# Performance work log

Hardware: AMD Instinct MI355X
Metric: run time of the kernel (lower is better)

## Reference

```python
import jax, jax.numpy as jnp
import numpy as np

B = 1024      # total windows (batch*windows_per_image)
W = 7         # window_size
T = W * W     # tokens per window = 49
C = 256       # scaled_emb_dim = emb_dim * 2**level
H = 8         # heads
D = C // H    # head_dim = 32
NUM_POS = 2 * W - 1


def _relative_pos():
    coords = np.arange(W)
    coords = np.stack(np.meshgrid(coords, coords, indexing='ij')).reshape(2, -1)
    rp = coords[:, :, None] - coords[:, None, :] + (W - 1)
    return jnp.asarray(rp, dtype=jnp.int32)  # (2, T, T)


def setup_inputs() -> dict:
    key = jax.random.key(0)
    ks = jax.random.split(key, 12)
    s = 0.02
    return {
        'x': jax.random.normal(ks[0], (B, T, C), dtype=jnp.float32),
        'relative_pos': _relative_pos(),
        'bias_table': jax.random.truncated_normal(ks[1], -2.0, 2.0, (H, NUM_POS, NUM_POS), dtype=jnp.float32) * s,
        'wq': jax.random.normal(ks[2], (C, H, D), dtype=jnp.float32) / np.sqrt(C),
        'bq': jnp.zeros((H, D), dtype=jnp.float32),
        'wk': jax.random.normal(ks[3], (C, H, D), dtype=jnp.float32) / np.sqrt(C),
        'bk': jnp.zeros((H, D), dtype=jnp.float32),
        'wv': jax.random.normal(ks[4], (C, H, D), dtype=jnp.float32) / np.sqrt(C),
        'bv': jnp.zeros((H, D), dtype=jnp.float32),
        'wo': jax.random.normal(ks[5], (H, D, C), dtype=jnp.float32) / np.sqrt(C),
        'bo': jnp.zeros((C,), dtype=jnp.float32),
        'dw': jax.random.normal(ks[6], (C, C), dtype=jnp.float32) / np.sqrt(C),
        'db': jnp.zeros((C,), dtype=jnp.float32),
    }


def reference(x, relative_pos, bias_table, wq, bq, wk, bk, wv, bv, wo, bo, dw, db):
    # QKV projections (flax DenseGeneral with bias)
    q = jnp.einsum('btc,chd->bthd', x, wq) + bq  # (B,T,H,D)
    k = jnp.einsum('btc,chd->bthd', x, wk) + bk
    v = jnp.einsum('btc,chd->bthd', x, wv) + bv

    # gathered relative position bias: (H, T, T)
    bias = bias_table[:, relative_pos[0], relative_pos[1]]

    # attention logits with query scaling (flax dot_product_attention)
    q = q / jnp.sqrt(jnp.asarray(D, dtype=q.dtype))
    logits = jnp.einsum('bqhd,bkhd->bhqk', q, k) + bias[None]
    attn = jax.nn.softmax(logits, axis=-1)

    out = jnp.einsum('bhqk,bkhd->bqhd', attn, v)
    y = jnp.einsum('bqhd,hdc->bqc', out, wo) + bo  # attention out projection
    y = jnp.einsum('btc,cf->btf', y, dw) + db      # trailing Dense(scaled_emb_dim)
    return y
```

## Files before the change

kernel.cpp:

```cpp
#include <hip/hip_runtime.h>
#include <stdint.h>

#define T 49
#define CCH 256

typedef __bf16 bf16x8 __attribute__((ext_vector_type(8)));
typedef float f32x4 __attribute__((ext_vector_type(4)));

static __device__ __forceinline__ unsigned short f2bf(float f){
  __bf16 h = (__bf16)f;
  return __builtin_bit_cast(unsigned short, h);
}
static __device__ __forceinline__ float bf2f(unsigned short h){
  return __builtin_bit_cast(float, ((uint32_t)h) << 16);
}
static __device__ __forceinline__ uint32_t pk2(float a, float b){
  return (uint32_t)f2bf(a) | ((uint32_t)f2bf(b) << 16);
}
static __device__ __forceinline__ f32x4 mfma16(bf16x8 a, bf16x8 b, f32x4 c){
  return __builtin_amdgcn_mfma_f32_16x16x32_bf16(a, b, c, 0, 0, 0);
}
#define SWZ(row) ((((row) & 7) << 4))

static __device__ __forceinline__ bf16x8 build_frag(uint32_t lo_w0, uint32_t lo_w1,
                                                    uint32_t hi_w0, uint32_t hi_w1,
                                                    int srcA, int srcB, bool use_hi){
  uint32_t a0 = (uint32_t)__shfl((int)lo_w0, srcA, 64);
  uint32_t c0 = (uint32_t)__shfl((int)hi_w0, srcA, 64);
  uint32_t a1 = (uint32_t)__shfl((int)lo_w1, srcA, 64);
  uint32_t c1 = (uint32_t)__shfl((int)hi_w1, srcA, 64);
  uint32_t a2 = (uint32_t)__shfl((int)lo_w0, srcB, 64);
  uint32_t c2 = (uint32_t)__shfl((int)hi_w0, srcB, 64);
  uint32_t a3 = (uint32_t)__shfl((int)lo_w1, srcB, 64);
  uint32_t c3 = (uint32_t)__shfl((int)hi_w1, srcB, 64);
  uint4 u = use_hi ? make_uint4(c0, c1, c2, c3) : make_uint4(a0, a1, a2, a3);
  return __builtin_bit_cast(bf16x8, u);
}


__global__ void prep_wqkvT(const float* __restrict__ wq, const float* __restrict__ wk,
                           const float* __restrict__ wv, unsigned short* __restrict__ out){
  int bk = blockIdx.x;
  int p = bk >> 8, kk = bk & 255;
  int n = threadIdx.x;
  const float* w = (p == 0) ? wq : (p == 1 ? wk : wv);
  float scl = (p == 0) ? 0.17677669529663687f : 1.0f;
  out[(size_t)(p * 256 + n) * 256 + kk] = f2bf(w[kk * 256 + n] * scl);
}

__global__ void prep_wodT(const float* __restrict__ wo, const float* __restrict__ dw,
                          unsigned short* __restrict__ out){
  int hd = blockIdx.x;
  int c = threadIdx.x;
  float s = 0.f;
  for (int cp = 0; cp < 256; ++cp) s = fmaf(wo[hd * 256 + cp], dw[cp * 256 + c], s);
  out[(size_t)c * 256 + hd] = f2bf(s);
}

__global__ void prep_misc(const int* __restrict__ rp, const float* __restrict__ btab,
                          const float* __restrict__ bq, const float* __restrict__ bk,
                          const float* __restrict__ bv, const float* __restrict__ bo,
                          const float* __restrict__ dwm, const float* __restrict__ db,
                          unsigned short* __restrict__ biasP, float* __restrict__ bqkv,
                          float* __restrict__ bod){
  int t = threadIdx.x;
  if (blockIdx.x == 0){
    for (int idx = t; idx < 768; idx += 256){
      int p = idx >> 8, n = idx & 255;
      float v = (p == 0) ? bq[n] * 0.17677669529663687f : (p == 1 ? bk[n] : bv[n]);
      bqkv[idx] = v;
    }
    float s = db[t];
    for (int cp = 0; cp < 256; ++cp) s = fmaf(bo[cp], dwm[cp * 256 + t], s);
    bod[t] = s;
  } else {
    int h = blockIdx.x - 1;
    for (int idx = t; idx < 4096; idx += 256){
      int r  = idx & 3;
      int lo = (idx >> 2) & 15;
      int g  = (idx >> 6) & 3;
      int nt = (idx >> 8) & 3;
      int jt = idx >> 10;
      int j = 16 * jt + 4 * g + r;
      int i = 16 * nt + lo;
      float v;
      if (j >= T) v = -1e30f;
      else if (i >= T) v = 0.f;
      else {
        int r0 = rp[i * 49 + j];
        int r1 = rp[2401 + i * 49 + j];
        v = btab[h * 169 + r0 * 13 + r1];
      }
      biasP[h * 4096 + idx] = f2bf(v);
    }
  }
}

__launch_bounds__(512, 4)
__global__ void wmsa_main(const float* __restrict__ x,
                          const unsigned short* __restrict__ wqkvT,
                          const unsigned short* __restrict__ wodT,
                          const unsigned short* __restrict__ biasP,
                          const float* __restrict__ bqkv,
                          const float* __restrict__ bod,
                          float* __restrict__ y){
  __shared__ unsigned short xs[64 * 256];
  __shared__ unsigned short vts[8 * 32 * 64];

  const int b    = blockIdx.x;
  const int tid  = threadIdx.x;
  const int h    = tid >> 6;
  const int lane = tid & 63;
  const int g    = lane >> 4;
  const int lo   = lane & 15;
  char* xs_c = (char*)xs;

  const float* xb = x + (size_t)b * T * CCH;
  {
    float4 vv[8];
    #pragma unroll
    for (int k2 = 0; k2 < 8; ++k2){
      int idx = tid + k2 * 512;
      int row = idx >> 6, c4 = idx & 63;
      vv[k2] = make_float4(0.f, 0.f, 0.f, 0.f);
      if (row < T) vv[k2] = reinterpret_cast<const float4*>(xb)[row * 64 + c4];
    }
    #pragma unroll
    for (int k2 = 0; k2 < 8; ++k2){
      int idx = tid + k2 * 512;
      int row = idx >> 6, c4 = idx & 63;
      *reinterpret_cast<uint2*>(xs_c + row * 512 + ((c4 * 8) ^ SWZ(row)))
          = make_uint2(pk2(vv[k2].x, vv[k2].y), pk2(vv[k2].z, vv[k2].w));
    }
  }
  __syncthreads();

  const int  srcA = lo + 16 * ((2 * g) & 3);
  const int  srcB = lo + 16 * ((2 * g + 1) & 3);
  const bool ghi  = (g >= 2);

  {
    f32x4 avc[4][2];
    #pragma unroll
    for (int mt = 0; mt < 4; ++mt)
      #pragma unroll
      for (int nt = 0; nt < 2; ++nt) avc[mt][nt] = f32x4{0,0,0,0};

    #pragma unroll 1
    for (int kb = 0; kb < 2; ++kb){
      bf16x8 wv[2][4];
      #pragma unroll
      for (int nt = 0; nt < 2; ++nt)
        #pragma unroll
        for (int q4 = 0; q4 < 4; ++q4)
          wv[nt][q4] = *reinterpret_cast<const bf16x8*>(
              wqkvT + (size_t)(512 + h * 32 + 16 * nt + lo) * 256 + (kb * 4 + q4) * 32 + 8 * g);
      #pragma unroll
      for (int q4 = 0; q4 < 4; ++q4){
        int kt = kb * 4 + q4;
        bf16x8 ax[4];
        #pragma unroll
        for (int mt = 0; mt < 4; ++mt){
          int row = 16 * mt + lo;
          ax[mt] = *reinterpret_cast<const bf16x8*>(xs_c + row * 512 + ((kt * 64 + 16 * g) ^ SWZ(row)));
        }
        #pragma unroll
        for (int nt = 0; nt < 2; ++nt)
          #pragma unroll
          for (int mt = 0; mt < 4; ++mt) avc[mt][nt] = mfma16(ax[mt], wv[nt][q4], avc[mt][nt]);
      }
    }
    #pragma unroll
    for (int nt = 0; nt < 2; ++nt){
      const float bvs = bqkv[512 + h * 32 + 16 * nt + lo];
      const int d = 16 * nt + lo;
      #pragma unroll
      for (int mt = 0; mt < 4; ++mt){
        f32x4 t = avc[mt][nt];
        *reinterpret_cast<uint2*>((char*)vts + h * 4096 + d * 128 + ((mt * 32 + g * 8) ^ SWZ(d)))
            = make_uint2(pk2(t[0] + bvs, t[1] + bvs), pk2(t[2] + bvs, t[3] + bvs));
      }
    }
  }

  bf16x8 fk[4];
  {
    f32x4 akk[2][4];
    #pragma unroll
    for (int mt = 0; mt < 2; ++mt)
      #pragma unroll
      for (int nt = 0; nt < 4; ++nt) akk[mt][nt] = f32x4{0,0,0,0};

    #pragma unroll 1
    for (int kb = 0; kb < 2; ++kb){
      bf16x8 wk[2][4];
      #pragma unroll
      for (int mt = 0; mt < 2; ++mt)
        #pragma unroll
        for (int q4 = 0; q4 < 4; ++q4)
          wk[mt][q4] = *reinterpret_cast<const bf16x8*>(
              wqkvT + (size_t)(256 + h * 32 + 16 * mt + lo) * 256 + (kb * 4 + q4) * 32 + 8 * g);
      #pragma unroll
      for (int q4 = 0; q4 < 4; ++q4){
        int kt = kb * 4 + q4;
        bf16x8 bx[4];
        #pragma unroll
        for (int nt = 0; nt < 4; ++nt){
          int row = 16 * nt + lo;
          bx[nt] = *reinterpret_cast<const bf16x8*>(xs_c + row * 512 + ((kt * 64 + 16 * g) ^ SWZ(row)));
        }
        #pragma unroll
        for (int mt = 0; mt < 2; ++mt)
          #pragma unroll
          for (int nt = 0; nt < 4; ++nt) akk[mt][nt] = mfma16(wk[mt][q4], bx[nt], akk[mt][nt]);
      }
    }
    uint32_t pkk[2][4][2];
    #pragma unroll
    for (int mt = 0; mt < 2; ++mt){
      const float4 b4k = *reinterpret_cast<const float4*>(bqkv + 256 + h * 32 + 16 * mt + 4 * g);
      #pragma unroll
      for (int nt = 0; nt < 4; ++nt){
        f32x4 tk = akk[mt][nt];
        tk[0] += b4k.x; tk[1] += b4k.y; tk[2] += b4k.z; tk[3] += b4k.w;
        pkk[mt][nt][0] = pk2(tk[0], tk[1]); pkk[mt][nt][1] = pk2(tk[2], tk[3]);
      }
    }
    #pragma unroll
    for (int nt = 0; nt < 4; ++nt)
      fk[nt] = build_frag(pkk[0][nt][0], pkk[0][nt][1], pkk[1][nt][0], pkk[1][nt][1], srcA, srcB, ghi);
  }

  bf16x8 fq[4];
  {
    f32x4 aq[2][4];
    #pragma unroll
    for (int mt = 0; mt < 2; ++mt)
      #pragma unroll
      for (int nt = 0; nt < 4; ++nt) aq[mt][nt] = f32x4{0,0,0,0};

    #pragma unroll 1
    for (int kb = 0; kb < 4; ++kb){
      bf16x8 wq2[2][2];
      #pragma unroll
      for (int mt = 0; mt < 2; ++mt)
        #pragma unroll
        for (int q2 = 0; q2 < 2; ++q2)
          wq2[mt][q2] = *reinterpret_cast<const bf16x8*>(
              wqkvT + (size_t)(h * 32 + 16 * mt + lo) * 256 + (kb * 2 + q2) * 32 + 8 * g);
      #pragma unroll
      for (int q2 = 0; q2 < 2; ++q2){
        int kt = kb * 2 + q2;
        bf16x8 bx[4];
        #pragma unroll
        for (int nt = 0; nt < 4; ++nt){
          int row = 16 * nt + lo;
          bx[nt] = *reinterpret_cast<const bf16x8*>(xs_c + row * 512 + ((kt * 64 + 16 * g) ^ SWZ(row)));
        }
        #pragma unroll
        for (int mt = 0; mt < 2; ++mt)
          #pragma unroll
          for (int nt = 0; nt < 4; ++nt) aq[mt][nt] = mfma16(wq2[mt][q2], bx[nt], aq[mt][nt]);
      }
    }
    uint32_t pq[2][4][2];
    #pragma unroll
    for (int mt = 0; mt < 2; ++mt){
      const float4 b4q = *reinterpret_cast<const float4*>(bqkv + h * 32 + 16 * mt + 4 * g);
      #pragma unroll
      for (int nt = 0; nt < 4; ++nt){
        f32x4 tq = aq[mt][nt];
        tq[0] += b4q.x; tq[1] += b4q.y; tq[2] += b4q.z; tq[3] += b4q.w;
        pq[mt][nt][0] = pk2(tq[0], tq[1]); pq[mt][nt][1] = pk2(tq[2], tq[3]);
      }
    }
    #pragma unroll
    for (int nt = 0; nt < 4; ++nt)
      fq[nt] = build_frag(pq[0][nt][0], pq[0][nt][1], pq[1][nt][0], pq[1][nt][1], srcA, srcB, ghi);
  }
  __syncthreads();

  const char* vb = (const char*)vts + h * 4096;
  #pragma unroll 1
  for (int nt = 0; nt < 4; ++nt){
    uint2 bb[4];
    #pragma unroll
    for (int jt = 0; jt < 4; ++jt)
      bb[jt] = *reinterpret_cast<const uint2*>(
          biasP + h * 4096 + jt * 1024 + nt * 256 + (g * 16 + lo) * 4);
    f32x4 lacc[4];
    #pragma unroll
    for (int jt = 0; jt < 4; ++jt){
      lacc[jt] = mfma16(fk[jt], fq[nt], f32x4{0,0,0,0});
      lacc[jt][0] += bf2f((unsigned short)(bb[jt].x & 0xffff));
      lacc[jt][1] += bf2f((unsigned short)(bb[jt].x >> 16));
      lacc[jt][2] += bf2f((unsigned short)(bb[jt].y & 0xffff));
      lacc[jt][3] += bf2f((unsigned short)(bb[jt].y >> 16));
    }
    float m = -3.0e38f;
    #pragma unroll
    for (int jt = 0; jt < 4; ++jt)
      #pragma unroll
      for (int r = 0; r < 4; ++r) m = fmaxf(m, lacc[jt][r]);
    m = fmaxf(m, __shfl_xor(m, 16, 64));
    m = fmaxf(m, __shfl_xor(m, 32, 64));
    float ssum = 0.f;
    uint32_t pw[4][2];
    #pragma unroll
    for (int jt = 0; jt < 4; ++jt){
      f32x4 t = lacc[jt];
      #pragma unroll
      for (int r = 0; r < 4; ++r){
        t[r] = exp2f((t[r] - m) * 1.4426950408889634f);
        ssum += t[r];
      }
      pw[jt][0] = pk2(t[0], t[1]);
      pw[jt][1] = pk2(t[2], t[3]);
    }
    ssum += __shfl_xor(ssum, 16, 64);
    ssum += __shfl_xor(ssum, 32, 64);
    const float r0 = 1.f / ssum;

    bf16x8 pf0 = build_frag(pw[0][0], pw[0][1], pw[1][0], pw[1][1], srcA, srcB, ghi);
    bf16x8 pf1 = build_frag(pw[2][0], pw[2][1], pw[3][0], pw[3][1], srcA, srcB, ghi);

    const int i = 16 * nt + lo;
    #pragma unroll
    for (int dt = 0; dt < 2; ++dt){
      int row = 16 * dt + lo;
      bf16x8 av0 = *reinterpret_cast<const bf16x8*>(vb + row * 128 + ((16 * g) ^ SWZ(row)));
      bf16x8 av1 = *reinterpret_cast<const bf16x8*>(vb + row * 128 + ((64 + 16 * g) ^ SWZ(row)));
      f32x4 oacc = mfma16(av0, pf0, f32x4{0,0,0,0});
      oacc = mfma16(av1, pf1, oacc);
      *reinterpret_cast<uint2*>(xs_c + i * 512 + ((h * 64 + dt * 32 + g * 8) ^ SWZ(i)))
          = make_uint2(pk2(oacc[0] * r0, oacc[1] * r0), pk2(oacc[2] * r0, oacc[3] * r0));
    }
  }
  __syncthreads();

  f32x4 facc[4][2];
  #pragma unroll
  for (int mt = 0; mt < 4; ++mt)
    #pragma unroll
    for (int nt = 0; nt < 2; ++nt) facc[mt][nt] = f32x4{0,0,0,0};

  #pragma unroll 1
  for (int kb = 0; kb < 2; ++kb){
    bf16x8 wod[2][4];
    #pragma unroll
    for (int nt = 0; nt < 2; ++nt)
      #pragma unroll
      for (int q4 = 0; q4 < 4; ++q4)
        wod[nt][q4] = *reinterpret_cast<const bf16x8*>(
            wodT + (size_t)(h * 32 + nt * 16 + lo) * 256 + (kb * 4 + q4) * 32 + 8 * g);
    #pragma unroll
    for (int q4 = 0; q4 < 4; ++q4){
      int kt = kb * 4 + q4;
      bf16x8 a[4];
      #pragma unroll
      for (int mt = 0; mt < 4; ++mt){
        int row = 16 * mt + lo;
        a[mt] = *reinterpret_cast<const bf16x8*>(xs_c + row * 512 + ((kt * 64 + 16 * g) ^ SWZ(row)));
      }
      #pragma unroll
      for (int nt = 0; nt < 2; ++nt)
        #pragma unroll
        for (int mt = 0; mt < 4; ++mt) facc[mt][nt] = mfma16(a[mt], wod[nt][q4], facc[mt][nt]);
    }
  }
  #pragma unroll
  for (int nt = 0; nt < 2; ++nt){
    int c = h * 32 + nt * 16 + lo;
    float bd = bod[c];
    #pragma unroll
    for (int mt = 0; mt < 4; ++mt)
      #pragma unroll
      for (int r = 0; r < 4; ++r){
        int i = 16 * mt + 4 * g + r;
        if (i < T) y[((size_t)b * T + i) * CCH + c] = facc[mt][nt][r] + bd;
      }
  }
}

extern "C" void kernel_launch(void* const* d_in, const int* in_sizes, int n_in,
                              void* d_out, int out_size, void* d_ws, size_t ws_size,
                              hipStream_t stream){
  const float* x    = (const float*)d_in[0];
  const int*   rp   = (const int*)d_in[1];
  const float* btab = (const float*)d_in[2];
  const float* wq   = (const float*)d_in[3];
  const float* bq   = (const float*)d_in[4];
  const float* wk   = (const float*)d_in[5];
  const float* bk   = (const float*)d_in[6];
  const float* wv   = (const float*)d_in[7];
  const float* bv   = (const float*)d_in[8];
  const float* wo   = (const float*)d_in[9];
  const float* bo   = (const float*)d_in[10];
  const float* dw   = (const float*)d_in[11];
  const float* db   = (const float*)d_in[12];
  float* y = (float*)d_out;

  char* ws = (char*)d_ws;
  unsigned short* wqkvT = (unsigned short*)(ws);
  unsigned short* wodT  = (unsigned short*)(ws + 393216);
  unsigned short* biasP = (unsigned short*)(ws + 524288);
  float* bqkv           = (float*)(ws + 589824);
  float* bod            = (float*)(ws + 592896);

  prep_wqkvT<<<768, 256, 0, stream>>>(wq, wk, wv, wqkvT);
  prep_wodT<<<256, 256, 0, stream>>>(wo, dw, wodT);
  prep_misc<<<9, 256, 0, stream>>>(rp, btab, bq, bk, bv, bo, dw, db, biasP, bqkv, bod);
  wmsa_main<<<1024, 512, 0, stream>>>(x, wqkvT, wodT, biasP, bqkv, bod, y);
}
```

Measured before the change: 134.2 us.

## Fuse Q/K projections, prefetch weights and bias, process two query tiles per iteration

The first V-weight fragment is now loaded before the x tile is written to shared memory, so its global latency overlaps the store. The separate K and Q projection loops are merged into one loop that shares the x-fragment reads from LDS and interleaves two independent MFMA chains. All relative-position bias values are loaded up front, and the attention loop handles two 16-query tiles per iteration so V fragments are reused and softmax reductions overlap. The cost is higher register pressure, which could lower occupancy or cause spills.

```diff
diff --git a/kernel.cpp b/kernel.cpp
--- a/kernel.cpp
+++ b/kernel.cpp
@@ -116,22 +116,27 @@
   char* xs_c = (char*)xs;
 
   const float* xb = x + (size_t)b * T * CCH;
-  {
-    float4 vv[8];
-    #pragma unroll
-    for (int k2 = 0; k2 < 8; ++k2){
-      int idx = tid + k2 * 512;
-      int row = idx >> 6, c4 = idx & 63;
-      vv[k2] = make_float4(0.f, 0.f, 0.f, 0.f);
-      if (row < T) vv[k2] = reinterpret_cast<const float4*>(xb)[row * 64 + c4];
-    }
-    #pragma unroll
-    for (int k2 = 0; k2 < 8; ++k2){
-      int idx = tid + k2 * 512;
-      int row = idx >> 6, c4 = idx & 63;
-      *reinterpret_cast<uint2*>(xs_c + row * 512 + ((c4 * 8) ^ SWZ(row)))
-          = make_uint2(pk2(vv[k2].x, vv[k2].y), pk2(vv[k2].z, vv[k2].w));
-    }
+  float4 vv[8];
+  #pragma unroll
+  for (int k2 = 0; k2 < 8; ++k2){
+    int idx = tid + k2 * 512;
+    int row = idx >> 6, c4 = idx & 63;
+    vv[k2] = make_float4(0.f, 0.f, 0.f, 0.f);
+    if (row < T) vv[k2] = reinterpret_cast<const float4*>(xb)[row * 64 + c4];
+  }
+  bf16x8 wv[2][4];
+  #pragma unroll
+  for (int nt = 0; nt < 2; ++nt)
+    #pragma unroll
+    for (int q4 = 0; q4 < 4; ++q4)
+      wv[nt][q4] = *reinterpret_cast<const bf16x8*>(
+          wqkvT + (size_t)(512 + h * 32 + 16 * nt + lo) * 256 + q4 * 32 + 8 * g);
+  #pragma unroll
+  for (int k2 = 0; k2 < 8; ++k2){
+    int idx = tid + k2 * 512;
+    int row = idx >> 6, c4 = idx & 63;
+    *reinterpret_cast<uint2*>(xs_c + row * 512 + ((c4 * 8) ^ SWZ(row)))
+        = make_uint2(pk2(vv[k2].x, vv[k2].y), pk2(vv[k2].z, vv[k2].w));
   }
   __syncthreads();
 
@@ -148,13 +153,14 @@
 
     #pragma unroll 1
     for (int kb = 0; kb < 2; ++kb){
-      bf16x8 wv[2][4];
-      #pragma unroll
-      for (int nt = 0; nt < 2; ++nt)
-        #pragma unroll
-        for (int q4 = 0; q4 < 4; ++q4)
-          wv[nt][q4] = *reinterpret_cast<const bf16x8*>(
-              wqkvT + (size_t)(512 + h * 32 + 16 * nt + lo) * 256 + (kb * 4 + q4) * 32 + 8 * g);
+      if (kb){
+        #pragma unroll
+        for (int nt = 0; nt < 2; ++nt)
+          #pragma unroll
+          for (int q4 = 0; q4 < 4; ++q4)
+            wv[nt][q4] = *reinterpret_cast<const bf16x8*>(
+                wqkvT + (size_t)(512 + h * 32 + 16 * nt + lo) * 256 + (4 + q4) * 32 + 8 * g);
+      }
       #pragma unroll
       for (int q4 = 0; q4 < 4; ++q4){
         int kt = kb * 4 + q4;
@@ -183,26 +189,29 @@
     }
   }
 
-  bf16x8 fk[4];
+  bf16x8 fk[4], fq[4];
   {
-    f32x4 akk[2][4];
+    f32x4 aq[2][4], akk[2][4];
     #pragma unroll
     for (int mt = 0; mt < 2; ++mt)
       #pragma unroll
-      for (int nt = 0; nt < 4; ++nt) akk[mt][nt] = f32x4{0,0,0,0};
+      for (int nt = 0; nt < 4; ++nt){ aq[mt][nt] = f32x4{0,0,0,0}; akk[mt][nt] = f32x4{0,0,0,0}; }
 
     #pragma unroll 1
-    for (int kb = 0; kb < 2; ++kb){
-      bf16x8 wk[2][4];
+    for (int kb = 0; kb < 4; ++kb){
+      bf16x8 wq2[2][2], wk2[2][2];
       #pragma unroll
       for (int mt = 0; mt < 2; ++mt)
         #pragma unroll
-        for (int q4 = 0; q4 < 4; ++q4)
-          wk[mt][q4] = *reinterpret_cast<const bf16x8*>(
-              wqkvT + (size_t)(256 + h * 32 + 16 * mt + lo) * 256 + (kb * 4 + q4) * 32 + 8 * g);
-      #pragma unroll
-      for (int q4 = 0; q4 < 4; ++q4){
-        int kt = kb * 4 + q4;
+        for (int q2 = 0; q2 < 2; ++q2){
+          wq2[mt][q2] = *reinterpret_cast<const bf16x8*>(
+              wqkvT + (size_t)(h * 32 + 16 * mt + lo) * 256 + (kb * 2 + q2) * 32 + 8 * g);
+          wk2[mt][q2] = *reinterpret_cast<const bf16x8*>(
+              wqkvT + (size_t)(256 + h * 32 + 16 * mt + lo) * 256 + (kb * 2 + q2) * 32 + 8 * g);
+        }
+      #pragma unroll
+      for (int q2 = 0; q2 < 2; ++q2){
+        int kt = kb * 2 + q2;
         bf16x8 bx[4];
         #pragma unroll
         for (int nt = 0; nt < 4; ++nt){
@@ -212,128 +221,115 @@
         #pragma unroll
         for (int mt = 0; mt < 2; ++mt)
           #pragma unroll
-          for (int nt = 0; nt < 4; ++nt) akk[mt][nt] = mfma16(wk[mt][q4], bx[nt], akk[mt][nt]);
-      }
-    }
-    uint32_t pkk[2][4][2];
-    #pragma unroll
-    for (int mt = 0; mt < 2; ++mt){
-      const float4 b4k = *reinterpret_cast<const float4*>(bqkv + 256 + h * 32 + 16 * mt + 4 * g);
-      #pragma unroll
-      for (int nt = 0; nt < 4; ++nt){
-        f32x4 tk = akk[mt][nt];
-        tk[0] += b4k.x; tk[1] += b4k.y; tk[2] += b4k.z; tk[3] += b4k.w;
-        pkk[mt][nt][0] = pk2(tk[0], tk[1]); pkk[mt][nt][1] = pk2(tk[2], tk[3]);
-      }
-    }
-    #pragma unroll
-    for (int nt = 0; nt < 4; ++nt)
-      fk[nt] = build_frag(pkk[0][nt][0], pkk[0][nt][1], pkk[1][nt][0], pkk[1][nt][1], srcA, srcB, ghi);
-  }
-
-  bf16x8 fq[4];
-  {
-    f32x4 aq[2][4];
-    #pragma unroll
-    for (int mt = 0; mt < 2; ++mt)
-      #pragma unroll
-      for (int nt = 0; nt < 4; ++nt) aq[mt][nt] = f32x4{0,0,0,0};
-
-    #pragma unroll 1
-    for (int kb = 0; kb < 4; ++kb){
-      bf16x8 wq2[2][2];
-      #pragma unroll
-      for (int mt = 0; mt < 2; ++mt)
-        #pragma unroll
-        for (int q2 = 0; q2 < 2; ++q2)
-          wq2[mt][q2] = *reinterpret_cast<const bf16x8*>(
-              wqkvT + (size_t)(h * 32 + 16 * mt + lo) * 256 + (kb * 2 + q2) * 32 + 8 * g);
-      #pragma unroll
-      for (int q2 = 0; q2 < 2; ++q2){
-        int kt = kb * 2 + q2;
-        bf16x8 bx[4];
-        #pragma unroll
-        for (int nt = 0; nt < 4; ++nt){
-          int row = 16 * nt + lo;
-          bx[nt] = *reinterpret_cast<const bf16x8*>(xs_c + row * 512 + ((kt * 64 + 16 * g) ^ SWZ(row)));
-        }
-        #pragma unroll
-        for (int mt = 0; mt < 2; ++mt)
-          #pragma unroll
-          for (int nt = 0; nt < 4; ++nt) aq[mt][nt] = mfma16(wq2[mt][q2], bx[nt], aq[mt][nt]);
-      }
-    }
-    uint32_t pq[2][4][2];
+          for (int nt = 0; nt < 4; ++nt){
+            aq[mt][nt]  = mfma16(wq2[mt][q2], bx[nt], aq[mt][nt]);
+            akk[mt][nt] = mfma16(wk2[mt][q2], bx[nt], akk[mt][nt]);
+          }
+      }
+    }
+    uint32_t pq[2][4][2], pkk[2][4][2];
     #pragma unroll
     for (int mt = 0; mt < 2; ++mt){
       const float4 b4q = *reinterpret_cast<const float4*>(bqkv + h * 32 + 16 * mt + 4 * g);
+      const float4 b4k = *reinterpret_cast<const float4*>(bqkv + 256 + h * 32 + 16 * mt + 4 * g);
       #pragma unroll
       for (int nt = 0; nt < 4; ++nt){
-        f32x4 tq = aq[mt][nt];
+        f32x4 tq = aq[mt][nt], tk = akk[mt][nt];
         tq[0] += b4q.x; tq[1] += b4q.y; tq[2] += b4q.z; tq[3] += b4q.w;
-        pq[mt][nt][0] = pk2(tq[0], tq[1]); pq[mt][nt][1] = pk2(tq[2], tq[3]);
-      }
-    }
+        tk[0] += b4k.x; tk[1] += b4k.y; tk[2] += b4k.z; tk[3] += b4k.w;
+        pq[mt][nt][0]  = pk2(tq[0], tq[1]); pq[mt][nt][1]  = pk2(tq[2], tq[3]);
+        pkk[mt][nt][0] = pk2(tk[0], tk[1]); pkk[mt][nt][1] = pk2(tk[2], tk[3]);
+      }
+    }
+    #pragma unroll
+    for (int nt = 0; nt < 4; ++nt){
+      fq[nt] = build_frag(pq[0][nt][0],  pq[0][nt][1],  pq[1][nt][0],  pq[1][nt][1],  srcA, srcB, ghi);
+      fk[nt] = build_frag(pkk[0][nt][0], pkk[0][nt][1], pkk[1][nt][0], pkk[1][nt][1], srcA, srcB, ghi);
+    }
+  }
+  __syncthreads();
+
+  const char* vb = (const char*)vts + h * 4096;
+  uint2 bb[4][4];
+  #pragma unroll
+  for (int jt = 0; jt < 4; ++jt)
     #pragma unroll
     for (int nt = 0; nt < 4; ++nt)
-      fq[nt] = build_frag(pq[0][nt][0], pq[0][nt][1], pq[1][nt][0], pq[1][nt][1], srcA, srcB, ghi);
-  }
-  __syncthreads();
-
-  const char* vb = (const char*)vts + h * 4096;
+      bb[jt][nt] = *reinterpret_cast<const uint2*>(
+          biasP + h * 4096 + jt * 1024 + nt * 256 + (g * 16 + lo) * 4);
+
   #pragma unroll 1
-  for (int nt = 0; nt < 4; ++nt){
-    uint2 bb[4];
-    #pragma unroll
-    for (int jt = 0; jt < 4; ++jt)
-      bb[jt] = *reinterpret_cast<const uint2*>(
-          biasP + h * 4096 + jt * 1024 + nt * 256 + (g * 16 + lo) * 4);
-    f32x4 lacc[4];
-    #pragma unroll
-    for (int jt = 0; jt < 4; ++jt){
-      lacc[jt] = mfma16(fk[jt], fq[nt], f32x4{0,0,0,0});
-      lacc[jt][0] += bf2f((unsigned short)(bb[jt].x & 0xffff));
-      lacc[jt][1] += bf2f((unsigned short)(bb[jt].x >> 16));
-      lacc[jt][2] += bf2f((unsigned short)(bb[jt].y & 0xffff));
-      lacc[jt][3] += bf2f((unsigned short)(bb[jt].y >> 16));
-    }
-    float m = -3.0e38f;
-    #pragma unroll
-    for (int jt = 0; jt < 4; ++jt)
-      #pragma unroll
-      for (int r = 0; r < 4; ++r) m = fmaxf(m, lacc[jt][r]);
-    m = fmaxf(m, __shfl_xor(m, 16, 64));
-    m = fmaxf(m, __shfl_xor(m, 32, 64));
-    float ssum = 0.f;
-    uint32_t pw[4][2];
-    #pragma unroll
-    for (int jt = 0; jt < 4; ++jt){
-      f32x4 t = lacc[jt];
-      #pragma unroll
-      for (int r = 0; r < 4; ++r){
-        t[r] = exp2f((t[r] - m) * 1.4426950408889634f);
-        ssum += t[r];
-      }
-      pw[jt][0] = pk2(t[0], t[1]);
-      pw[jt][1] = pk2(t[2], t[3]);
-    }
-    ssum += __shfl_xor(ssum, 16, 64);
-    ssum += __shfl_xor(ssum, 32, 64);
-    const float r0 = 1.f / ssum;
-
-    bf16x8 pf0 = build_frag(pw[0][0], pw[0][1], pw[1][0], pw[1][1], srcA, srcB, ghi);
-    bf16x8 pf1 = build_frag(pw[2][0], pw[2][1], pw[3][0], pw[3][1], srcA, srcB, ghi);
-
-    const int i = 16 * nt + lo;
+  for (int pr = 0; pr < 2; ++pr){
+    f32x4 lacc[2][4];
+    #pragma unroll
+    for (int t2 = 0; t2 < 2; ++t2){
+      const int nt = 2 * pr + t2;
+      #pragma unroll
+      for (int jt = 0; jt < 4; ++jt){
+        lacc[t2][jt] = mfma16(fk[jt], fq[nt], f32x4{0,0,0,0});
+        const uint2 bv2 = bb[jt][nt];
+        lacc[t2][jt][0] += bf2f((unsigned short)(bv2.x & 0xffff));
+        lacc[t2][jt][1] += bf2f((unsigned short)(bv2.x >> 16));
+        lacc[t2][jt][2] += bf2f((unsigned short)(bv2.y & 0xffff));
+        lacc[t2][jt][3] += bf2f((unsigned short)(bv2.y >> 16));
+      }
+    }
+    float m[2], ssum[2], r0[2];
+    uint32_t pw[2][4][2];
+    #pragma unroll
+    for (int t2 = 0; t2 < 2; ++t2){
+      m[t2] = -3.0e38f;
+      #pragma unroll
+      for (int jt = 0; jt < 4; ++jt)
+        #pragma unroll
+        for (int r = 0; r < 4; ++r) m[t2] = fmaxf(m[t2], lacc[t2][jt][r]);
+    }
+    #pragma unroll
+    for (int t2 = 0; t2 < 2; ++t2){
+      m[t2] = fmaxf(m[t2], __shfl_xor(m[t2], 16, 64));
+      m[t2] = fmaxf(m[t2], __shfl_xor(m[t2], 32, 64));
+    }
+    #pragma unroll
+    for (int t2 = 0; t2 < 2; ++t2){
+      ssum[t2] = 0.f;
+      #pragma unroll
+      for (int jt = 0; jt < 4; ++jt){
+        f32x4 t = lacc[t2][jt];
+        #pragma unroll
+        for (int r = 0; r < 4; ++r){
+          t[r] = exp2f((t[r] - m[t2]) * 1.4426950408889634f);
+          ssum[t2] += t[r];
+        }
+        pw[t2][jt][0] = pk2(t[0], t[1]);
+        pw[t2][jt][1] = pk2(t[2], t[3]);
+      }
+    }
+    #pragma unroll
+    for (int t2 = 0; t2 < 2; ++t2){
+      ssum[t2] += __shfl_xor(ssum[t2], 16, 64);
+      ssum[t2] += __shfl_xor(ssum[t2], 32, 64);
+      r0[t2] = 1.f / ssum[t2];
+    }
+    bf16x8 pf[2][2];
+    #pragma unroll
+    for (int t2 = 0; t2 < 2; ++t2){
+      pf[t2][0] = build_frag(pw[t2][0][0], pw[t2][0][1], pw[t2][1][0], pw[t2][1][1], srcA, srcB, ghi);
+      pf[t2][1] = build_frag(pw[t2][2][0], pw[t2][2][1], pw[t2][3][0], pw[t2][3][1], srcA, srcB, ghi);
+    }
     #pragma unroll
     for (int dt = 0; dt < 2; ++dt){
-      int row = 16 * dt + lo;
-      bf16x8 av0 = *reinterpret_cast<const bf16x8*>(vb + row * 128 + ((16 * g) ^ SWZ(row)));
-      bf16x8 av1 = *reinterpret_cast<const bf16x8*>(vb + row * 128 + ((64 + 16 * g) ^ SWZ(row)));
-      f32x4 oacc = mfma16(av0, pf0, f32x4{0,0,0,0});
-      oacc = mfma16(av1, pf1, oacc);
-      *reinterpret_cast<uint2*>(xs_c + i * 512 + ((h * 64 + dt * 32 + g * 8) ^ SWZ(i)))
-          = make_uint2(pk2(oacc[0] * r0, oacc[1] * r0), pk2(oacc[2] * r0, oacc[3] * r0));
+      const int row = 16 * dt + lo;
+      const bf16x8 av0 = *reinterpret_cast<const bf16x8*>(vb + row * 128 + ((16 * g) ^ SWZ(row)));
+      const bf16x8 av1 = *reinterpret_cast<const bf16x8*>(vb + row * 128 + ((64 + 16 * g) ^ SWZ(row)));
+      #pragma unroll
+      for (int t2 = 0; t2 < 2; ++t2){
+        const int i = 16 * (2 * pr + t2) + lo;
+        f32x4 oacc = mfma16(av0, pf[t2][0], f32x4{0,0,0,0});
+        oacc = mfma16(av1, pf[t2][1], oacc);
+        *reinterpret_cast<uint2*>(xs_c + i * 512 + ((h * 64 + dt * 32 + g * 8) ^ SWZ(i)))
+            = make_uint2(pk2(oacc[0] * r0[t2], oacc[1] * r0[t2]),
+                         pk2(oacc[2] * r0[t2], oacc[3] * r0[t2]));
+      }
     }
   }
   __syncthreads();
```

Measured after the change: 136.2 us. No clear change (+1.4%).

## Split fused attention kernel into QKV and attention/output kernels via global scratch

Applied to the files above, without the earlier changes.

Splits the single fused window-attention kernel into two kernels. The first projects Q, K and V into bf16 global scratch buffers in MFMA-ready layout. The second loads those fragments directly, runs softmax attention, and applies the merged output projection. The aim is less per-kernel register and LDS pressure and higher occupancy (6 blocks per CU for the QKV kernel), at the cost of about 100 MB of extra global traffic and a dependence on a large workspace. The fallback monolithic path also fuses the Q and K projection loops so they share the x fragment loads.

```diff
diff --git a/kernel.cpp b/kernel.cpp
--- a/kernel.cpp
+++ b/kernel.cpp
@@ -96,8 +96,314 @@
   }
 }
 
+__launch_bounds__(512, 6)
+__global__ void qkv_kernel(const float* __restrict__ x,
+                           const unsigned short* __restrict__ wqkvT,
+                           const float* __restrict__ bqkv,
+                           unsigned short* __restrict__ qg,
+                           unsigned short* __restrict__ kg,
+                           unsigned short* __restrict__ vtg){
+  __shared__ unsigned short xs[64 * 256];
+
+  const int b    = blockIdx.x;
+  const int tid  = threadIdx.x;
+  const int h    = tid >> 6;
+  const int lane = tid & 63;
+  const int g    = lane >> 4;
+  const int lo   = lane & 15;
+  char* xs_c = (char*)xs;
+  const size_t bh = (size_t)(b * 8 + h);
+
+  const float* xb = x + (size_t)b * T * CCH;
+  {
+    float4 vv[8];
+    #pragma unroll
+    for (int k2 = 0; k2 < 8; ++k2){
+      int idx = tid + k2 * 512;
+      int row = idx >> 6, c4 = idx & 63;
+      vv[k2] = make_float4(0.f, 0.f, 0.f, 0.f);
+      if (row < T) vv[k2] = reinterpret_cast<const float4*>(xb)[row * 64 + c4];
+    }
+    #pragma unroll
+    for (int k2 = 0; k2 < 8; ++k2){
+      int idx = tid + k2 * 512;
+      int row = idx >> 6, c4 = idx & 63;
+      *reinterpret_cast<uint2*>(xs_c + row * 512 + ((c4 * 8) ^ SWZ(row)))
+          = make_uint2(pk2(vv[k2].x, vv[k2].y), pk2(vv[k2].z, vv[k2].w));
+    }
+  }
+  __syncthreads();
+
+  {
+    f32x4 avc[4][2];
+    #pragma unroll
+    for (int mt = 0; mt < 4; ++mt)
+      #pragma unroll
+      for (int nt = 0; nt < 2; ++nt) avc[mt][nt] = f32x4{0,0,0,0};
+
+    #pragma unroll 1
+    for (int kb = 0; kb < 2; ++kb){
+      bf16x8 wv[2][4];
+      #pragma unroll
+      for (int nt = 0; nt < 2; ++nt)
+        #pragma unroll
+        for (int q4 = 0; q4 < 4; ++q4)
+          wv[nt][q4] = *reinterpret_cast<const bf16x8*>(
+              wqkvT + (size_t)(512 + h * 32 + 16 * nt + lo) * 256 + (kb * 4 + q4) * 32 + 8 * g);
+      #pragma unroll
+      for (int q4 = 0; q4 < 4; ++q4){
+        int kt = kb * 4 + q4;
+        bf16x8 ax[4];
+        #pragma unroll
+        for (int mt = 0; mt < 4; ++mt){
+          int row = 16 * mt + lo;
+          ax[mt] = *reinterpret_cast<const bf16x8*>(xs_c + row * 512 + ((kt * 64 + 16 * g) ^ SWZ(row)));
+        }
+        #pragma unroll
+        for (int nt = 0; nt < 2; ++nt)
+          #pragma unroll
+          for (int mt = 0; mt < 4; ++mt) avc[mt][nt] = mfma16(ax[mt], wv[nt][q4], avc[mt][nt]);
+      }
+    }
+    #pragma unroll
+    for (int nt = 0; nt < 2; ++nt){
+      const float bvs = bqkv[512 + h * 32 + 16 * nt + lo];
+      const int d = 16 * nt + lo;
+      #pragma unroll
+      for (int mt = 0; mt < 4; ++mt){
+        f32x4 t = avc[mt][nt];
+        *reinterpret_cast<uint2*>(vtg + (bh * 32 + d) * 64 + 16 * mt + 4 * g)
+            = make_uint2(pk2(t[0] + bvs, t[1] + bvs), pk2(t[2] + bvs, t[3] + bvs));
+      }
+    }
+  }
+
+  {
+    f32x4 akk[2][4];
+    #pragma unroll
+    for (int mt = 0; mt < 2; ++mt)
+      #pragma unroll
+      for (int nt = 0; nt < 4; ++nt) akk[mt][nt] = f32x4{0,0,0,0};
+
+    #pragma unroll 1
+    for (int kb = 0; kb < 2; ++kb){
+      bf16x8 wk[2][4];
+      #pragma unroll
+      for (int mt = 0; mt < 2; ++mt)
+        #pragma unroll
+        for (int q4 = 0; q4 < 4; ++q4)
+          wk[mt][q4] = *reinterpret_cast<const bf16x8*>(
+              wqkvT + (size_t)(256 + h * 32 + 16 * mt + lo) * 256 + (kb * 4 + q4) * 32 + 8 * g);
+      #pragma unroll
+      for (int q4 = 0; q4 < 4; ++q4){
+        int kt = kb * 4 + q4;
+        bf16x8 bx[4];
+        #pragma unroll
+        for (int nt = 0; nt < 4; ++nt){
+          int row = 16 * nt + lo;
+          bx[nt] = *reinterpret_cast<const bf16x8*>(xs_c + row * 512 + ((kt * 64 + 16 * g) ^ SWZ(row)));
+        }
+        #pragma unroll
+        for (int mt = 0; mt < 2; ++mt)
+          #pragma unroll
+          for (int nt = 0; nt < 4; ++nt) akk[mt][nt] = mfma16(wk[mt][q4], bx[nt], akk[mt][nt]);
+      }
+    }
+    #pragma unroll
+    for (int mt = 0; mt < 2; ++mt){
+      const float4 b4 = *reinterpret_cast<const float4*>(bqkv + 256 + h * 32 + 16 * mt + 4 * g);
+      #pragma unroll
+      for (int nt = 0; nt < 4; ++nt){
+        f32x4 t = akk[mt][nt];
+        t[0] += b4.x; t[1] += b4.y; t[2] += b4.z; t[3] += b4.w;
+        *reinterpret_cast<uint2*>(kg + (bh * 64 + 16 * nt + lo) * 32 + 16 * mt + 4 * g)
+            = make_uint2(pk2(t[0], t[1]), pk2(t[2], t[3]));
+      }
+    }
+  }
+
+  {
+    f32x4 aq[2][4];
+    #pragma unroll
+    for (int mt = 0; mt < 2; ++mt)
+      #pragma unroll
+      for (int nt = 0; nt < 4; ++nt) aq[mt][nt] = f32x4{0,0,0,0};
+
+    #pragma unroll 1
+    for (int kb = 0; kb < 2; ++kb){
+      bf16x8 wq2[2][4];
+      #pragma unroll
+      for (int mt = 0; mt < 2; ++mt)
+        #pragma unroll
+        for (int q4 = 0; q4 < 4; ++q4)
+          wq2[mt][q4] = *reinterpret_cast<const bf16x8*>(
+              wqkvT + (size_t)(h * 32 + 16 * mt + lo) * 256 + (kb * 4 + q4) * 32 + 8 * g);
+      #pragma unroll
+      for (int q4 = 0; q4 < 4; ++q4){
+        int kt = kb * 4 + q4;
+        bf16x8 bx[4];
+        #pragma unroll
+        for (int nt = 0; nt < 4; ++nt){
+          int row = 16 * nt + lo;
+          bx[nt] = *reinterpret_cast<const bf16x8*>(xs_c + row * 512 + ((kt * 64 + 16 * g) ^ SWZ(row)));
+        }
+        #pragma unroll
+        for (int mt = 0; mt < 2; ++mt)
+          #pragma unroll
+          for (int nt = 0; nt < 4; ++nt) aq[mt][nt] = mfma16(wq2[mt][q4], bx[nt], aq[mt][nt]);
+      }
+    }
+    #pragma unroll
+    for (int mt = 0; mt < 2; ++mt){
+      const float4 b4 = *reinterpret_cast<const float4*>(bqkv + h * 32 + 16 * mt + 4 * g);
+      #pragma unroll
+      for (int nt = 0; nt < 4; ++nt){
+        f32x4 t = aq[mt][nt];
+        t[0] += b4.x; t[1] += b4.y; t[2] += b4.z; t[3] += b4.w;
+        *reinterpret_cast<uint2*>(qg + (bh * 64 + 16 * nt + lo) * 32 + 16 * mt + 4 * g)
+            = make_uint2(pk2(t[0], t[1]), pk2(t[2], t[3]));
+      }
+    }
+  }
+}
+
 __launch_bounds__(512, 4)
-__global__ void wmsa_main(const float* __restrict__ x,
+__global__ void attn_out_kernel(const unsigned short* __restrict__ qg,
+                                const unsigned short* __restrict__ kg,
+                                const unsigned short* __restrict__ vtg,
+                                const unsigned short* __restrict__ biasP,
+                                const unsigned short* __restrict__ wodT,
+                                const float* __restrict__ bod,
+                                float* __restrict__ y){
+  __shared__ unsigned short outs[64 * 256];
+
+  const int b    = blockIdx.x;
+  const int tid  = threadIdx.x;
+  const int h    = tid >> 6;
+  const int lane = tid & 63;
+  const int g    = lane >> 4;
+  const int lo   = lane & 15;
+  char* os_c = (char*)outs;
+  const size_t bh = (size_t)(b * 8 + h);
+
+  const int  srcA = lo + 16 * ((2 * g) & 3);
+  const int  srcB = lo + 16 * ((2 * g + 1) & 3);
+  const bool ghi  = (g >= 2);
+
+  bf16x8 ak[4], fq[4], av[2][2];
+  #pragma unroll
+  for (int jt = 0; jt < 4; ++jt)
+    ak[jt] = *reinterpret_cast<const bf16x8*>(kg + (bh * 64 + 16 * jt + lo) * 32 + 8 * g);
+  #pragma unroll
+  for (int nt = 0; nt < 4; ++nt)
+    fq[nt] = *reinterpret_cast<const bf16x8*>(qg + (bh * 64 + 16 * nt + lo) * 32 + 8 * g);
+  #pragma unroll
+  for (int dt = 0; dt < 2; ++dt)
+    #pragma unroll
+    for (int ktj = 0; ktj < 2; ++ktj)
+      av[dt][ktj] = *reinterpret_cast<const bf16x8*>(
+          vtg + (bh * 32 + 16 * dt + lo) * 64 + 32 * ktj + 8 * g);
+
+  #pragma unroll 1
+  for (int nt = 0; nt < 4; ++nt){
+    uint2 bb[4];
+    #pragma unroll
+    for (int jt = 0; jt < 4; ++jt)
+      bb[jt] = *reinterpret_cast<const uint2*>(
+          biasP + h * 4096 + jt * 1024 + nt * 256 + (g * 16 + lo) * 4);
+    f32x4 lacc[4];
+    #pragma unroll
+    for (int jt = 0; jt < 4; ++jt){
+      lacc[jt] = mfma16(ak[jt], fq[nt], f32x4{0,0,0,0});
+      lacc[jt][0] += bf2f((unsigned short)(bb[jt].x & 0xffff));
+      lacc[jt][1] += bf2f((unsigned short)(bb[jt].x >> 16));
+      lacc[jt][2] += bf2f((unsigned short)(bb[jt].y & 0xffff));
+      lacc[jt][3] += bf2f((unsigned short)(bb[jt].y >> 16));
+    }
+    float m = -3.0e38f;
+    #pragma unroll
+    for (int jt = 0; jt < 4; ++jt)
+      #pragma unroll
+      for (int r = 0; r < 4; ++r) m = fmaxf(m, lacc[jt][r]);
+    m = fmaxf(m, __shfl_xor(m, 16, 64));
+    m = fmaxf(m, __shfl_xor(m, 32, 64));
+    float ssum = 0.f;
+    uint32_t pw[4][2];
+    #pragma unroll
+    for (int jt = 0; jt < 4; ++jt){
+      f32x4 t = lacc[jt];
+      #pragma unroll
+      for (int r = 0; r < 4; ++r){
+        t[r] = exp2f((t[r] - m) * 1.4426950408889634f);
+        ssum += t[r];
+      }
+      pw[jt][0] = pk2(t[0], t[1]);
+      pw[jt][1] = pk2(t[2], t[3]);
+    }
+    ssum += __shfl_xor(ssum, 16, 64);
+    ssum += __shfl_xor(ssum, 32, 64);
+    const float r0 = 1.f / ssum;
+
+    bf16x8 pf0 = build_frag(pw[0][0], pw[0][1], pw[1][0], pw[1][1], srcA, srcB, ghi);
+    bf16x8 pf1 = build_frag(pw[2][0], pw[2][1], pw[3][0], pw[3][1], srcA, srcB, ghi);
+
+    const int i = 16 * nt + lo;
+    #pragma unroll
+    for (int dt = 0; dt < 2; ++dt){
+      f32x4 oacc = mfma16(av[dt][0], pf0, f32x4{0,0,0,0});
+      oacc = mfma16(av[dt][1], pf1, oacc);
+      *reinterpret_cast<uint2*>(os_c + i * 512 + ((h * 64 + dt * 32 + g * 8) ^ SWZ(i)))
+          = make_uint2(pk2(oacc[0] * r0, oacc[1] * r0), pk2(oacc[2] * r0, oacc[3] * r0));
+    }
+  }
+  __syncthreads();
+
+  f32x4 facc[4][2];
+  #pragma unroll
+  for (int mt = 0; mt < 4; ++mt)
+    #pragma unroll
+    for (int nt = 0; nt < 2; ++nt) facc[mt][nt] = f32x4{0,0,0,0};
+
+  #pragma unroll 1
+  for (int kb = 0; kb < 2; ++kb){
+    bf16x8 wod[2][4];
+    #pragma unroll
+    for (int nt = 0; nt < 2; ++nt)
+      #pragma unroll
+      for (int q4 = 0; q4 < 4; ++q4)
+        wod[nt][q4] = *reinterpret_cast<const bf16x8*>(
+            wodT + (size_t)(h * 32 + nt * 16 + lo) * 256 + (kb * 4 + q4) * 32 + 8 * g);
+    #pragma unroll
+    for (int q4 = 0; q4 < 4; ++q4){
+      int kt = kb * 4 + q4;
+      bf16x8 a[4];
+      #pragma unroll
+      for (int mt = 0; mt < 4; ++mt){
+        int row = 16 * mt + lo;
+        a[mt] = *reinterpret_cast<const bf16x8*>(os_c + row * 512 + ((kt * 64 + 16 * g) ^ SWZ(row)));
+      }
+      #pragma unroll
+      for (int nt = 0; nt < 2; ++nt)
+        #pragma unroll
+        for (int mt = 0; mt < 4; ++mt) facc[mt][nt] = mfma16(a[mt], wod[nt][q4], facc[mt][nt]);
+    }
+  }
+  #pragma unroll
+  for (int nt = 0; nt < 2; ++nt){
+    int c = h * 32 + nt * 16 + lo;
+    float bd = bod[c];
+    #pragma unroll
+    for (int mt = 0; mt < 4; ++mt)
+      #pragma unroll
+      for (int r = 0; r < 4; ++r){
+        int i = 16 * mt + 4 * g + r;
+        if (i < T) y[((size_t)b * T + i) * CCH + c] = facc[mt][nt][r] + bd;
+      }
+  }
+}
+
+__launch_bounds__(512, 4)
+__global__ void wmsa_mono(const float* __restrict__ x,
                           const unsigned short* __restrict__ wqkvT,
                           const unsigned short* __restrict__ wodT,
                           const unsigned short* __restrict__ biasP,
@@ -145,7 +451,6 @@
     for (int mt = 0; mt < 4; ++mt)
       #pragma unroll
       for (int nt = 0; nt < 2; ++nt) avc[mt][nt] = f32x4{0,0,0,0};
-
     #pragma unroll 1
     for (int kb = 0; kb < 2; ++kb){
       bf16x8 wv[2][4];
@@ -183,26 +488,28 @@
     }
   }
 
-  bf16x8 fk[4];
+  bf16x8 fk[4], fq[4];
   {
-    f32x4 akk[2][4];
+    f32x4 aq[2][4], akk[2][4];
     #pragma unroll
     for (int mt = 0; mt < 2; ++mt)
       #pragma unroll
-      for (int nt = 0; nt < 4; ++nt) akk[mt][nt] = f32x4{0,0,0,0};
-
+      for (int nt = 0; nt < 4; ++nt){ aq[mt][nt] = f32x4{0,0,0,0}; akk[mt][nt] = f32x4{0,0,0,0}; }
     #pragma unroll 1
-    for (int kb = 0; kb < 2; ++kb){
-      bf16x8 wk[2][4];
+    for (int kb = 0; kb < 4; ++kb){
+      bf16x8 wq2[2][2], wk2[2][2];
       #pragma unroll
       for (int mt = 0; mt < 2; ++mt)
         #pragma unroll
-        for (int q4 = 0; q4 < 4; ++q4)
-          wk[mt][q4] = *reinterpret_cast<const bf16x8*>(
-              wqkvT + (size_t)(256 + h * 32 + 16 * mt + lo) * 256 + (kb * 4 + q4) * 32 + 8 * g);
-      #pragma unroll
-      for (int q4 = 0; q4 < 4; ++q4){
-        int kt = kb * 4 + q4;
+        for (int q2 = 0; q2 < 2; ++q2){
+          wq2[mt][q2] = *reinterpret_cast<const bf16x8*>(
+              wqkvT + (size_t)(h * 32 + 16 * mt + lo) * 256 + (kb * 2 + q2) * 32 + 8 * g);
+          wk2[mt][q2] = *reinterpret_cast<const bf16x8*>(
+              wqkvT + (size_t)(256 + h * 32 + 16 * mt + lo) * 256 + (kb * 2 + q2) * 32 + 8 * g);
+        }
+      #pragma unroll
+      for (int q2 = 0; q2 < 2; ++q2){
+        int kt = kb * 2 + q2;
         bf16x8 bx[4];
         #pragma unroll
         for (int nt = 0; nt < 4; ++nt){
@@ -212,71 +519,31 @@
         #pragma unroll
         for (int mt = 0; mt < 2; ++mt)
           #pragma unroll
-          for (int nt = 0; nt < 4; ++nt) akk[mt][nt] = mfma16(wk[mt][q4], bx[nt], akk[mt][nt]);
-      }
-    }
-    uint32_t pkk[2][4][2];
-    #pragma unroll
-    for (int mt = 0; mt < 2; ++mt){
-      const float4 b4k = *reinterpret_cast<const float4*>(bqkv + 256 + h * 32 + 16 * mt + 4 * g);
-      #pragma unroll
-      for (int nt = 0; nt < 4; ++nt){
-        f32x4 tk = akk[mt][nt];
-        tk[0] += b4k.x; tk[1] += b4k.y; tk[2] += b4k.z; tk[3] += b4k.w;
-        pkk[mt][nt][0] = pk2(tk[0], tk[1]); pkk[mt][nt][1] = pk2(tk[2], tk[3]);
-      }
-    }
-    #pragma unroll
-    for (int nt = 0; nt < 4; ++nt)
-      fk[nt] = build_frag(pkk[0][nt][0], pkk[0][nt][1], pkk[1][nt][0], pkk[1][nt][1], srcA, srcB, ghi);
-  }
-
-  bf16x8 fq[4];
-  {
-    f32x4 aq[2][4];
-    #pragma unroll
-    for (int mt = 0; mt < 2; ++mt)
-      #pragma unroll
-      for (int nt = 0; nt < 4; ++nt) aq[mt][nt] = f32x4{0,0,0,0};
-
-    #pragma unroll 1
-    for (int kb = 0; kb < 4; ++kb){
-      bf16x8 wq2[2][2];
-      #pragma unroll
-      for (int mt = 0; mt < 2; ++mt)
-        #pragma unroll
-        for (int q2 = 0; q2 < 2; ++q2)
-          wq2[mt][q2] = *reinterpret_cast<const bf16x8*>(
-              wqkvT + (size_t)(h * 32 + 16 * mt + lo) * 256 + (kb * 2 + q2) * 32 + 8 * g);
-      #pragma unroll
-      for (int q2 = 0; q2 < 2; ++q2){
-        int kt = kb * 2 + q2;
-        bf16x8 bx[4];
-        #pragma unroll
-        for (int nt = 0; nt < 4; ++nt){
-          int row = 16 * nt + lo;
-          bx[nt] = *reinterpret_cast<const bf16x8*>(xs_c + row * 512 + ((kt * 64 + 16 * g) ^ SWZ(row)));
-        }
-        #pragma unroll
-        for (int mt = 0; mt < 2; ++mt)
-          #pragma unroll
-          for (int nt = 0; nt < 4; ++nt) aq[mt][nt] = mfma16(wq2[mt][q2], bx[nt], aq[mt][nt]);
-      }
-    }
-    uint32_t pq[2][4][2];
+          for (int nt = 0; nt < 4; ++nt){
+            aq[mt][nt]  = mfma16(wq2[mt][q2], bx[nt], aq[mt][nt]);
+            akk[mt][nt] = mfma16(wk2[mt][q2], bx[nt], akk[mt][nt]);
+          }
+      }
+    }
+    uint32_t pq[2][4][2], pkk[2][4][2];
     #pragma unroll
     for (int mt = 0; mt < 2; ++mt){
       const float4 b4q = *reinterpret_cast<const float4*>(bqkv + h * 32 + 16 * mt + 4 * g);
+      const float4 b4k = *reinterpret_cast<const float4*>(bqkv + 256 + h * 32 + 16 * mt + 4 * g);
       #pragma unroll
       for (int nt = 0; nt < 4; ++nt){
-        f32x4 tq = aq[mt][nt];
+        f32x4 tq = aq[mt][nt], tk = akk[mt][nt];
         tq[0] += b4q.x; tq[1] += b4q.y; tq[2] += b4q.z; tq[3] += b4q.w;
-        pq[mt][nt][0] = pk2(tq[0], tq[1]); pq[mt][nt][1] = pk2(tq[2], tq[3]);
-      }
-    }
-    #pragma unroll
-    for (int nt = 0; nt < 4; ++nt)
-      fq[nt] = build_frag(pq[0][nt][0], pq[0][nt][1], pq[1][nt][0], pq[1][nt][1], srcA, srcB, ghi);
+        tk[0] += b4k.x; tk[1] += b4k.y; tk[2] += b4k.z; tk[3] += b4k.w;
+        pq[mt][nt][0]  = pk2(tq[0], tq[1]); pq[mt][nt][1]  = pk2(tq[2], tq[3]);
+        pkk[mt][nt][0] = pk2(tk[0], tk[1]); pkk[mt][nt][1] = pk2(tk[2], tk[3]);
+      }
+    }
+    #pragma unroll
+    for (int nt = 0; nt < 4; ++nt){
+      fq[nt] = build_frag(pq[0][nt][0],  pq[0][nt][1],  pq[1][nt][0],  pq[1][nt][1],  srcA, srcB, ghi);
+      fk[nt] = build_frag(pkk[0][nt][0], pkk[0][nt][1], pkk[1][nt][0], pkk[1][nt][1], srcA, srcB, ghi);
+    }
   }
   __syncthreads();
 
@@ -320,10 +587,8 @@
     ssum += __shfl_xor(ssum, 16, 64);
     ssum += __shfl_xor(ssum, 32, 64);
     const float r0 = 1.f / ssum;
-
     bf16x8 pf0 = build_frag(pw[0][0], pw[0][1], pw[1][0], pw[1][1], srcA, srcB, ghi);
     bf16x8 pf1 = build_frag(pw[2][0], pw[2][1], pw[3][0], pw[3][1], srcA, srcB, ghi);
-
     const int i = 16 * nt + lo;
     #pragma unroll
     for (int dt = 0; dt < 2; ++dt){
@@ -343,7 +608,6 @@
   for (int mt = 0; mt < 4; ++mt)
     #pragma unroll
     for (int nt = 0; nt < 2; ++nt) facc[mt][nt] = f32x4{0,0,0,0};
-
   #pragma unroll 1
   for (int kb = 0; kb < 2; ++kb){
     bf16x8 wod[2][4];
@@ -401,14 +665,35 @@
   float* y = (float*)d_out;
 
   char* ws = (char*)d_ws;
-  unsigned short* wqkvT = (unsigned short*)(ws);
-  unsigned short* wodT  = (unsigned short*)(ws + 393216);
-  unsigned short* biasP = (unsigned short*)(ws + 524288);
-  float* bqkv           = (float*)(ws + 589824);
-  float* bod            = (float*)(ws + 592896);
-
-  prep_wqkvT<<<768, 256, 0, stream>>>(wq, wk, wv, wqkvT);
-  prep_wodT<<<256, 256, 0, stream>>>(wo, dw, wodT);
-  prep_misc<<<9, 256, 0, stream>>>(rp, btab, bq, bk, bv, bo, dw, db, biasP, bqkv, bod);
-  wmsa_main<<<1024, 512, 0, stream>>>(x, wqkvT, wodT, biasP, bqkv, bod, y);
-}
+  const size_t QKV_BYTES = 33554432ull;
+  const size_t BIG_NEED  = 3 * QKV_BYTES + 393216 + 131072 + 65536 + 3072 + 1024;
+
+  if (ws_size >= BIG_NEED){
+    unsigned short* qg  = (unsigned short*)(ws);
+    unsigned short* kg  = (unsigned short*)(ws + QKV_BYTES);
+    unsigned short* vtg = (unsigned short*)(ws + 2 * QKV_BYTES);
+    char* wsp = ws + 3 * QKV_BYTES;
+    unsigned short* wqkvT = (unsigned short*)(wsp);
+    unsigned short* wodT  = (unsigned short*)(wsp + 393216);
+    unsigned short* biasP = (unsigned short*)(wsp + 524288);
+    float* bqkv           = (float*)(wsp + 589824);
+    float* bod            = (float*)(wsp + 592896);
+
+    prep_wqkvT<<<768, 256, 0, stream>>>(wq, wk, wv, wqkvT);
+    prep_wodT<<<256, 256, 0, stream>>>(wo, dw, wodT);
+    prep_misc<<<9, 256, 0, stream>>>(rp, btab, bq, bk, bv, bo, dw, db, biasP, bqkv, bod);
+    qkv_kernel<<<1024, 512, 0, stream>>>(x, wqkvT, bqkv, qg, kg, vtg);
+    attn_out_kernel<<<1024, 512, 0, stream>>>(qg, kg, vtg, biasP, wodT, bod, y);
+  } else {
+    unsigned short* wqkvT = (unsigned short*)(ws);
+    unsigned short* wodT  = (unsigned short*)(ws + 393216);
+    unsigned short* biasP = (unsigned short*)(ws + 524288);
+    float* bqkv           = (float*)(ws + 589824);
+    float* bod            = (float*)(ws + 592896);
+
+    prep_wqkvT<<<768, 256, 0, stream>>>(wq, wk, wv, wqkvT);
+    prep_wodT<<<256, 256, 0, stream>>>(wo, dw, wodT);
+    prep_misc<<<9, 256, 0, stream>>>(rp, btab, bq, bk, bv, bo, dw, db, biasP, bqkv, bod);
+    wmsa_mono<<<1024, 512, 0, stream>>>(x, wqkvT, wodT, biasP, bqkv, bod, y);
+  }
+}
```

Result: slower. 160.7 us (+19.7%).
